# Kernel optimization log

Measured on AMD Instinct MI355X. Metric: run time of the kernel, lower is better.

The kernel has to match this reference:

```python
import jax, jax.numpy as jnp
import numpy as np

N = 65536
SIZES = [3, 256, 256, 256, 256, 1]
NU = np.float32(0.01 / np.pi)  # viscosity coefficient 0.01/pi


def setup_inputs() -> dict:
    key = jax.random.key(0)
    ks = jax.random.split(key, 16)
    inp = {
        "t": jax.random.uniform(ks[0], (N, 1), dtype=jnp.float32),
        "x": jax.random.uniform(ks[1], (N, 1), dtype=jnp.float32),
        "y": jax.random.uniform(ks[2], (N, 1), dtype=jnp.float32),
    }
    for i in range(len(SIZES) - 1):
        fan_in, fan_out = SIZES[i], SIZES[i + 1]
        scale = jnp.float32(1.0 / np.sqrt(fan_in))
        inp[f"W{i}"] = jax.random.normal(ks[3 + i], (fan_in, fan_out), dtype=jnp.float32) * scale
        inp[f"b{i}"] = jnp.zeros((fan_out,), dtype=jnp.float32)
    return inp


def reference(t, x, y, W0, b0, W1, b1, W2, b2, W3, b3, W4, b4):
    Ws = (W0, W1, W2, W3, W4)
    bs = (b0, b1, b2, b3, b4)

    def u_scalar(pt):  # pt: (3,) -> scalar u(t,x,y)
        h = pt
        for W, b in zip(Ws[:-1], bs[:-1]):
            h = jnp.tanh(h @ W + b)
        return (h @ Ws[-1] + bs[-1])[0]

    def point(pt):
        u, g = jax.value_and_grad(u_scalar)(pt)          # g = (u_t, u_x, u_y)
        H = jax.jacfwd(jax.grad(u_scalar))(pt)           # 3x3 Hessian (fwd-over-rev)
        f = g[0] + u * g[1] + u * g[2] - NU * (H[1, 1] + H[2, 2])
        return u, f

    pts = jnp.concatenate((t, x, y), axis=1)  # [N, 3]
    u, f = jax.vmap(point)(pts)
    return u[:, None], f[:, None]
```

## Files before the change

kernel.cpp:

```cpp
#include <hip/hip_runtime.h>

#define NPTS 65536
#define NU_F 0.0031830988618379067f

typedef __attribute__((ext_vector_type(8)))  _Float16 half8v;
typedef __attribute__((ext_vector_type(16))) float    f32x16;

__device__ __forceinline__ void jet5(float z, float zt, float zx, float zy, float zl,
                                     float& s0, float& s1, float& s2, float& s3, float& s4) {
    float e  = __expf(2.0f * z);
    float a  = 1.0f - 2.0f * __builtin_amdgcn_rcpf(e + 1.0f);
    float ap = 1.0f - a * a;
    float am = -2.0f * a * ap;
    s0 = a;
    s1 = ap * zt;
    s2 = ap * zx;
    s3 = ap * zy;
    s4 = ap * zl + am * (zx * zx + zy * zy);
}

__device__ __forceinline__ int swzoff(int sp, int byteInRow) {
    return (sp << 9) + (byteInRow ^ ((sp & 31) << 4));
}
union h4u { ushort4 u4; _Float16 h[4]; };
__device__ __forceinline__ void storeJ(char* baseB, int sp, int j0,
                                       _Float16 a0, _Float16 a1, _Float16 a2, _Float16 a3) {
    h4u v; v.h[0] = a0; v.h[1] = a1; v.h[2] = a2; v.h[3] = a3;
    *(ushort4*)(baseB + swzoff(sp, j0 * 2)) = v.u4;
}

__global__ __launch_bounds__(256)
void pinn_prep_kernel(const float* __restrict__ W1, const float* __restrict__ W2,
                      const float* __restrict__ W3, _Float16* __restrict__ ws) {
    int gid  = blockIdx.x * 256 + threadIdx.x;
    int l    = gid >> 13;
    int rem  = gid & 8191;
    int M    = rem >> 10;
    int kt   = (rem >> 6) & 15;
    int lane = rem & 63;
    const float* W = (l == 0) ? W1 : (l == 1) ? W2 : W3;
    int j  = M * 32 + (lane & 31);
    int k0 = kt * 16 + (lane >> 5) * 8;
    union { _Float16 h[8]; half8v v; } hf;
    #pragma unroll
    for (int jj = 0; jj < 8; ++jj)
        hf.h[jj] = (_Float16)W[(k0 + jj) * 256 + j];
    ((half8v*)ws)[l * 8192 + (M * 16 + kt) * 64 + lane] = hf.v;
}

__global__ __launch_bounds__(256, 2)
void pinn_burger2d_kernel(
    const float* __restrict__ t, const float* __restrict__ x, const float* __restrict__ y,
    const float* __restrict__ W0, const float* __restrict__ b0,
    const float* __restrict__ b1, const float* __restrict__ b2, const float* __restrict__ b3,
    const float* __restrict__ W4, const float* __restrict__ b4,
    const _Float16* __restrict__ wf, float* __restrict__ out)
{
    __shared__ _Float16 BjS[5 * 32 * 256];
    char* bjB = (char*)BjS;

    const int tid  = threadIdx.x;
    const int lane = tid & 63;
    const int wv   = tid >> 6;
    const int p    = lane & 31;
    const int kg   = lane >> 5;
    const int base = blockIdx.x * 32;
    const int gi   = base + p;

    const float tv = t[gi], xv = x[gi], yv = y[gi];

    #pragma unroll
    for (int m = 0; m < 2; ++m) {
        #pragma unroll
        for (int q = 0; q < 4; ++q) {
            const int j0 = wv * 64 + m * 32 + kg * 16 + q * 4;
            float4 w0t = *(const float4*)(W0 + j0);
            float4 w0x = *(const float4*)(W0 + 256 + j0);
            float4 w0y = *(const float4*)(W0 + 512 + j0);
            float4 bb  = *(const float4*)(b0 + j0);
            float wtA[4] = {w0t.x, w0t.y, w0t.z, w0t.w};
            float wxA[4] = {w0x.x, w0x.y, w0x.z, w0x.w};
            float wyA[4] = {w0y.x, w0y.y, w0y.z, w0y.w};
            float bbA[4] = {bb.x, bb.y, bb.z, bb.w};
            _Float16 h[5][4];
            #pragma unroll
            for (int i = 0; i < 4; ++i) {
                float z = tv * wtA[i] + xv * wxA[i] + yv * wyA[i] + bbA[i];
                float s0, s1, s2, s3, s4;
                jet5(z, wtA[i], wxA[i], wyA[i], 0.0f, s0, s1, s2, s3, s4);
                h[0][i] = (_Float16)s0; h[1][i] = (_Float16)s1; h[2][i] = (_Float16)s2;
                h[3][i] = (_Float16)s3; h[4][i] = (_Float16)s4;
            }
            #pragma unroll
            for (int s = 0; s < 5; ++s)
                storeJ(bjB, s * 32 + p, j0, h[s][0], h[s][1], h[s][2], h[s][3]);
        }
    }
    __syncthreads();

    f32x16 acc[2][5];

    for (int li = 0; li < 3; ++li) {
        #pragma unroll
        for (int m = 0; m < 2; ++m)
            #pragma unroll
            for (int c = 0; c < 5; ++c)
                acc[m][c] = (f32x16)(0.0f);

        const half8v* whf = (const half8v*)wf + li * 8192;

        #pragma unroll 4
        for (int kt = 0; kt < 16; ++kt) {
            const int bRow = kt * 32 + kg * 16;
            half8v bv0 = *(const half8v*)(bjB + swzoff(       p, bRow));
            half8v bv1 = *(const half8v*)(bjB + swzoff( 32 + p, bRow));
            half8v bv2 = *(const half8v*)(bjB + swzoff( 64 + p, bRow));
            half8v bv3 = *(const half8v*)(bjB + swzoff( 96 + p, bRow));
            half8v bv4 = *(const half8v*)(bjB + swzoff(128 + p, bRow));
            const int fa = (wv * 32 + kt) * 64 + lane;
            half8v whA = whf[fa];
            half8v whB = whf[fa + 1024];
            acc[0][0] = __builtin_amdgcn_mfma_f32_32x32x16_f16(whA, bv0, acc[0][0], 0, 0, 0);
            acc[0][1] = __builtin_amdgcn_mfma_f32_32x32x16_f16(whA, bv1, acc[0][1], 0, 0, 0);
            acc[0][2] = __builtin_amdgcn_mfma_f32_32x32x16_f16(whA, bv2, acc[0][2], 0, 0, 0);
            acc[0][3] = __builtin_amdgcn_mfma_f32_32x32x16_f16(whA, bv3, acc[0][3], 0, 0, 0);
            acc[0][4] = __builtin_amdgcn_mfma_f32_32x32x16_f16(whA, bv4, acc[0][4], 0, 0, 0);
            acc[1][0] = __builtin_amdgcn_mfma_f32_32x32x16_f16(whB, bv0, acc[1][0], 0, 0, 0);
            acc[1][1] = __builtin_amdgcn_mfma_f32_32x32x16_f16(whB, bv1, acc[1][1], 0, 0, 0);
            acc[1][2] = __builtin_amdgcn_mfma_f32_32x32x16_f16(whB, bv2, acc[1][2], 0, 0, 0);
            acc[1][3] = __builtin_amdgcn_mfma_f32_32x32x16_f16(whB, bv3, acc[1][3], 0, 0, 0);
            acc[1][4] = __builtin_amdgcn_mfma_f32_32x32x16_f16(whB, bv4, acc[1][4], 0, 0, 0);
        }
        __syncthreads();

        if (li < 2) {
            const float* bL = (li == 0) ? b1 : b2;
            #pragma unroll
            for (int m = 0; m < 2; ++m) {
                const int jt = (wv * 2 + m) * 32;
                #pragma unroll
                for (int q = 0; q < 4; ++q) {
                    const int j0 = jt + 8 * q + 4 * kg;
                    float4 bb = *(const float4*)(bL + j0);
                    float bbA[4] = {bb.x, bb.y, bb.z, bb.w};
                    _Float16 h[5][4];
                    #pragma unroll
                    for (int i = 0; i < 4; ++i) {
                        const int r = 4 * q + i;
                        float s0, s1, s2, s3, s4;
                        jet5(acc[m][0][r] + bbA[i], acc[m][1][r], acc[m][2][r],
                             acc[m][3][r], acc[m][4][r], s0, s1, s2, s3, s4);
                        h[0][i] = (_Float16)s0; h[1][i] = (_Float16)s1; h[2][i] = (_Float16)s2;
                        h[3][i] = (_Float16)s3; h[4][i] = (_Float16)s4;
                    }
                    #pragma unroll
                    for (int s = 0; s < 5; ++s)
                        storeJ(bjB, s * 32 + p, j0, h[s][0], h[s][1], h[s][2], h[s][3]);
                }
            }
            __syncthreads();
        }
    }

    float part[5] = {0, 0, 0, 0, 0};
    #pragma unroll
    for (int m = 0; m < 2; ++m) {
        const int jt = (wv * 2 + m) * 32;
        #pragma unroll
        for (int q = 0; q < 4; ++q) {
            const int j0 = jt + 8 * q + 4 * kg;
            float4 bb = *(const float4*)(b3 + j0);
            float4 w4 = *(const float4*)(W4 + j0);
            float bbA[4] = {bb.x, bb.y, bb.z, bb.w};
            float w4A[4] = {w4.x, w4.y, w4.z, w4.w};
            #pragma unroll
            for (int i = 0; i < 4; ++i) {
                const int r = 4 * q + i;
                float s0, s1, s2, s3, s4;
                jet5(acc[m][0][r] + bbA[i], acc[m][1][r], acc[m][2][r],
                     acc[m][3][r], acc[m][4][r], s0, s1, s2, s3, s4);
                part[0] += s0 * w4A[i];
                part[1] += s1 * w4A[i];
                part[2] += s2 * w4A[i];
                part[3] += s3 * w4A[i];
                part[4] += s4 * w4A[i];
            }
        }
    }
    #pragma unroll
    for (int s = 0; s < 5; ++s) part[s] += __shfl_xor(part[s], 32, 64);

    float* resf = (float*)BjS;
    if (lane < 32) {
        #pragma unroll
        for (int s = 0; s < 5; ++s) resf[(wv * 5 + s) * 32 + p] = part[s];
    }
    __syncthreads();

    if (tid < 32) {
        const int pp = tid;
        const int g  = base + pp;
        float u = b4[0], ut = 0, ux = 0, uy = 0, lap = 0;
        #pragma unroll
        for (int w = 0; w < 4; ++w) {
            u   += resf[(w * 5 + 0) * 32 + pp];
            ut  += resf[(w * 5 + 1) * 32 + pp];
            ux  += resf[(w * 5 + 2) * 32 + pp];
            uy  += resf[(w * 5 + 3) * 32 + pp];
            lap += resf[(w * 5 + 4) * 32 + pp];
        }
        out[g]        = u;
        out[NPTS + g] = ut + u * ux + u * uy - NU_F * lap;
    }
}

extern "C" void kernel_launch(void* const* d_in, const int* in_sizes, int n_in,
                              void* d_out, int out_size, void* d_ws, size_t ws_size,
                              hipStream_t stream) {
    const float* t  = (const float*)d_in[0];
    const float* x  = (const float*)d_in[1];
    const float* y  = (const float*)d_in[2];
    const float* W0 = (const float*)d_in[3];
    const float* b0 = (const float*)d_in[4];
    const float* W1 = (const float*)d_in[5];
    const float* b1 = (const float*)d_in[6];
    const float* W2 = (const float*)d_in[7];
    const float* b2 = (const float*)d_in[8];
    const float* W3 = (const float*)d_in[9];
    const float* b3 = (const float*)d_in[10];
    const float* W4 = (const float*)d_in[11];
    const float* b4 = (const float*)d_in[12];
    float* out = (float*)d_out;

    pinn_prep_kernel<<<96, 256, 0, stream>>>(W1, W2, W3, (_Float16*)d_ws);
    pinn_burger2d_kernel<<<NPTS / 32, 256, 0, stream>>>(
        t, x, y, W0, b0, b1, b2, b3, W4, b4, (const _Float16*)d_ws, out);
}
```

Baseline: 136.4 us.

## Switch to 16x16x32 MFMA with 16 points per block and higher occupancy

Each block now handles 16 points instead of 32, and the per-layer matmuls use 16x16x32 MFMA tiles with four output tiles per wave. The weight prepack is rewritten to match the new fragment layout. Shared memory and accumulator registers are halved, so launch bounds now target 4 blocks per CU. The cost is that each weight fragment loaded from global memory is reused over fewer points, roughly doubling weight traffic per point, and the final reduction needs an extra shuffle.

```diff
diff --git a/kernel.cpp b/kernel.cpp
--- a/kernel.cpp
+++ b/kernel.cpp
@@ -3,8 +3,8 @@
 #define NPTS 65536
 #define NU_F 0.0031830988618379067f
 
-typedef __attribute__((ext_vector_type(8)))  _Float16 half8v;
-typedef __attribute__((ext_vector_type(16))) float    f32x16;
+typedef __attribute__((ext_vector_type(8))) _Float16 half8v;
+typedef __attribute__((ext_vector_type(4))) float    f32x4;
 
 __device__ __forceinline__ void jet5(float z, float zt, float zx, float zy, float zl,
                                      float& s0, float& s1, float& s2, float& s3, float& s4) {
@@ -35,20 +35,20 @@
     int gid  = blockIdx.x * 256 + threadIdx.x;
     int l    = gid >> 13;
     int rem  = gid & 8191;
-    int M    = rem >> 10;
-    int kt   = (rem >> 6) & 15;
+    int M    = rem >> 9;
+    int kt   = (rem >> 6) & 7;
     int lane = rem & 63;
     const float* W = (l == 0) ? W1 : (l == 1) ? W2 : W3;
-    int j  = M * 32 + (lane & 31);
-    int k0 = kt * 16 + (lane >> 5) * 8;
+    int j  = M * 16 + (lane & 15);
+    int k0 = kt * 32 + (lane >> 4) * 8;
     union { _Float16 h[8]; half8v v; } hf;
     #pragma unroll
     for (int jj = 0; jj < 8; ++jj)
         hf.h[jj] = (_Float16)W[(k0 + jj) * 256 + j];
-    ((half8v*)ws)[l * 8192 + (M * 16 + kt) * 64 + lane] = hf.v;
-}
-
-__global__ __launch_bounds__(256, 2)
+    ((half8v*)ws)[l * 8192 + (M * 8 + kt) * 64 + lane] = hf.v;
+}
+
+__global__ __launch_bounds__(256, 4)
 void pinn_burger2d_kernel(
     const float* __restrict__ t, const float* __restrict__ x, const float* __restrict__ y,
     const float* __restrict__ W0, const float* __restrict__ b0,
@@ -56,107 +56,95 @@
     const float* __restrict__ W4, const float* __restrict__ b4,
     const _Float16* __restrict__ wf, float* __restrict__ out)
 {
-    __shared__ _Float16 BjS[5 * 32 * 256];
+    __shared__ _Float16 BjS[5 * 16 * 256];
     char* bjB = (char*)BjS;
 
     const int tid  = threadIdx.x;
     const int lane = tid & 63;
     const int wv   = tid >> 6;
-    const int p    = lane & 31;
-    const int kg   = lane >> 5;
-    const int base = blockIdx.x * 32;
+    const int p    = lane & 15;
+    const int quad = lane >> 4;
+    const int base = blockIdx.x * 16;
     const int gi   = base + p;
 
     const float tv = t[gi], xv = x[gi], yv = y[gi];
 
     #pragma unroll
-    for (int m = 0; m < 2; ++m) {
-        #pragma unroll
-        for (int q = 0; q < 4; ++q) {
-            const int j0 = wv * 64 + m * 32 + kg * 16 + q * 4;
-            float4 w0t = *(const float4*)(W0 + j0);
-            float4 w0x = *(const float4*)(W0 + 256 + j0);
-            float4 w0y = *(const float4*)(W0 + 512 + j0);
-            float4 bb  = *(const float4*)(b0 + j0);
-            float wtA[4] = {w0t.x, w0t.y, w0t.z, w0t.w};
-            float wxA[4] = {w0x.x, w0x.y, w0x.z, w0x.w};
-            float wyA[4] = {w0y.x, w0y.y, w0y.z, w0y.w};
-            float bbA[4] = {bb.x, bb.y, bb.z, bb.w};
-            _Float16 h[5][4];
-            #pragma unroll
-            for (int i = 0; i < 4; ++i) {
-                float z = tv * wtA[i] + xv * wxA[i] + yv * wyA[i] + bbA[i];
-                float s0, s1, s2, s3, s4;
-                jet5(z, wtA[i], wxA[i], wyA[i], 0.0f, s0, s1, s2, s3, s4);
-                h[0][i] = (_Float16)s0; h[1][i] = (_Float16)s1; h[2][i] = (_Float16)s2;
-                h[3][i] = (_Float16)s3; h[4][i] = (_Float16)s4;
-            }
-            #pragma unroll
-            for (int s = 0; s < 5; ++s)
-                storeJ(bjB, s * 32 + p, j0, h[s][0], h[s][1], h[s][2], h[s][3]);
-        }
+    for (int m = 0; m < 4; ++m) {
+        const int j0 = wv * 64 + m * 16 + quad * 4;
+        float4 w0t = *(const float4*)(W0 + j0);
+        float4 w0x = *(const float4*)(W0 + 256 + j0);
+        float4 w0y = *(const float4*)(W0 + 512 + j0);
+        float4 bb  = *(const float4*)(b0 + j0);
+        float wtA[4] = {w0t.x, w0t.y, w0t.z, w0t.w};
+        float wxA[4] = {w0x.x, w0x.y, w0x.z, w0x.w};
+        float wyA[4] = {w0y.x, w0y.y, w0y.z, w0y.w};
+        float bbA[4] = {bb.x, bb.y, bb.z, bb.w};
+        _Float16 h[5][4];
+        #pragma unroll
+        for (int i = 0; i < 4; ++i) {
+            float z = tv * wtA[i] + xv * wxA[i] + yv * wyA[i] + bbA[i];
+            float s0, s1, s2, s3, s4;
+            jet5(z, wtA[i], wxA[i], wyA[i], 0.0f, s0, s1, s2, s3, s4);
+            h[0][i] = (_Float16)s0; h[1][i] = (_Float16)s1; h[2][i] = (_Float16)s2;
+            h[3][i] = (_Float16)s3; h[4][i] = (_Float16)s4;
+        }
+        #pragma unroll
+        for (int s = 0; s < 5; ++s)
+            storeJ(bjB, s * 16 + p, j0, h[s][0], h[s][1], h[s][2], h[s][3]);
     }
     __syncthreads();
 
-    f32x16 acc[2][5];
+    f32x4 acc[4][5];
 
     for (int li = 0; li < 3; ++li) {
         #pragma unroll
-        for (int m = 0; m < 2; ++m)
+        for (int m = 0; m < 4; ++m)
             #pragma unroll
             for (int c = 0; c < 5; ++c)
-                acc[m][c] = (f32x16)(0.0f);
+                acc[m][c] = (f32x4)(0.0f);
 
         const half8v* whf = (const half8v*)wf + li * 8192;
 
-        #pragma unroll 4
-        for (int kt = 0; kt < 16; ++kt) {
-            const int bRow = kt * 32 + kg * 16;
-            half8v bv0 = *(const half8v*)(bjB + swzoff(       p, bRow));
-            half8v bv1 = *(const half8v*)(bjB + swzoff( 32 + p, bRow));
-            half8v bv2 = *(const half8v*)(bjB + swzoff( 64 + p, bRow));
-            half8v bv3 = *(const half8v*)(bjB + swzoff( 96 + p, bRow));
-            half8v bv4 = *(const half8v*)(bjB + swzoff(128 + p, bRow));
-            const int fa = (wv * 32 + kt) * 64 + lane;
-            half8v whA = whf[fa];
-            half8v whB = whf[fa + 1024];
-            acc[0][0] = __builtin_amdgcn_mfma_f32_32x32x16_f16(whA, bv0, acc[0][0], 0, 0, 0);
-            acc[0][1] = __builtin_amdgcn_mfma_f32_32x32x16_f16(whA, bv1, acc[0][1], 0, 0, 0);
-            acc[0][2] = __builtin_amdgcn_mfma_f32_32x32x16_f16(whA, bv2, acc[0][2], 0, 0, 0);
-            acc[0][3] = __builtin_amdgcn_mfma_f32_32x32x16_f16(whA, bv3, acc[0][3], 0, 0, 0);
-            acc[0][4] = __builtin_amdgcn_mfma_f32_32x32x16_f16(whA, bv4, acc[0][4], 0, 0, 0);
-            acc[1][0] = __builtin_amdgcn_mfma_f32_32x32x16_f16(whB, bv0, acc[1][0], 0, 0, 0);
-            acc[1][1] = __builtin_amdgcn_mfma_f32_32x32x16_f16(whB, bv1, acc[1][1], 0, 0, 0);
-            acc[1][2] = __builtin_amdgcn_mfma_f32_32x32x16_f16(whB, bv2, acc[1][2], 0, 0, 0);
-            acc[1][3] = __builtin_amdgcn_mfma_f32_32x32x16_f16(whB, bv3, acc[1][3], 0, 0, 0);
-            acc[1][4] = __builtin_amdgcn_mfma_f32_32x32x16_f16(whB, bv4, acc[1][4], 0, 0, 0);
+        #pragma unroll 2
+        for (int kt = 0; kt < 8; ++kt) {
+            const int bRow = kt * 64 + quad * 16;
+            half8v bv0 = *(const half8v*)(bjB + swzoff(     p, bRow));
+            half8v bv1 = *(const half8v*)(bjB + swzoff(16 + p, bRow));
+            half8v bv2 = *(const half8v*)(bjB + swzoff(32 + p, bRow));
+            half8v bv3 = *(const half8v*)(bjB + swzoff(48 + p, bRow));
+            half8v bv4 = *(const half8v*)(bjB + swzoff(64 + p, bRow));
+            #pragma unroll
+            for (int m = 0; m < 4; ++m) {
+                half8v wh = whf[((wv * 4 + m) * 8 + kt) * 64 + lane];
+                acc[m][0] = __builtin_amdgcn_mfma_f32_16x16x32_f16(wh, bv0, acc[m][0], 0, 0, 0);
+                acc[m][1] = __builtin_amdgcn_mfma_f32_16x16x32_f16(wh, bv1, acc[m][1], 0, 0, 0);
+                acc[m][2] = __builtin_amdgcn_mfma_f32_16x16x32_f16(wh, bv2, acc[m][2], 0, 0, 0);
+                acc[m][3] = __builtin_amdgcn_mfma_f32_16x16x32_f16(wh, bv3, acc[m][3], 0, 0, 0);
+                acc[m][4] = __builtin_amdgcn_mfma_f32_16x16x32_f16(wh, bv4, acc[m][4], 0, 0, 0);
+            }
         }
         __syncthreads();
 
         if (li < 2) {
             const float* bL = (li == 0) ? b1 : b2;
             #pragma unroll
-            for (int m = 0; m < 2; ++m) {
-                const int jt = (wv * 2 + m) * 32;
+            for (int m = 0; m < 4; ++m) {
+                const int j0 = (wv * 4 + m) * 16 + quad * 4;
+                float4 bb = *(const float4*)(bL + j0);
+                float bbA[4] = {bb.x, bb.y, bb.z, bb.w};
+                _Float16 h[5][4];
                 #pragma unroll
-                for (int q = 0; q < 4; ++q) {
-                    const int j0 = jt + 8 * q + 4 * kg;
-                    float4 bb = *(const float4*)(bL + j0);
-                    float bbA[4] = {bb.x, bb.y, bb.z, bb.w};
-                    _Float16 h[5][4];
-                    #pragma unroll
-                    for (int i = 0; i < 4; ++i) {
-                        const int r = 4 * q + i;
-                        float s0, s1, s2, s3, s4;
-                        jet5(acc[m][0][r] + bbA[i], acc[m][1][r], acc[m][2][r],
-                             acc[m][3][r], acc[m][4][r], s0, s1, s2, s3, s4);
-                        h[0][i] = (_Float16)s0; h[1][i] = (_Float16)s1; h[2][i] = (_Float16)s2;
-                        h[3][i] = (_Float16)s3; h[4][i] = (_Float16)s4;
-                    }
-                    #pragma unroll
-                    for (int s = 0; s < 5; ++s)
-                        storeJ(bjB, s * 32 + p, j0, h[s][0], h[s][1], h[s][2], h[s][3]);
+                for (int i = 0; i < 4; ++i) {
+                    float s0, s1, s2, s3, s4;
+                    jet5(acc[m][0][i] + bbA[i], acc[m][1][i], acc[m][2][i],
+                         acc[m][3][i], acc[m][4][i], s0, s1, s2, s3, s4);
+                    h[0][i] = (_Float16)s0; h[1][i] = (_Float16)s1; h[2][i] = (_Float16)s2;
+                    h[3][i] = (_Float16)s3; h[4][i] = (_Float16)s4;
                 }
+                #pragma unroll
+                for (int s = 0; s < 5; ++s)
+                    storeJ(bjB, s * 16 + p, j0, h[s][0], h[s][1], h[s][2], h[s][3]);
             }
             __syncthreads();
         }
@@ -164,50 +152,48 @@
 
     float part[5] = {0, 0, 0, 0, 0};
     #pragma unroll
-    for (int m = 0; m < 2; ++m) {
-        const int jt = (wv * 2 + m) * 32;
-        #pragma unroll
-        for (int q = 0; q < 4; ++q) {
-            const int j0 = jt + 8 * q + 4 * kg;
-            float4 bb = *(const float4*)(b3 + j0);
-            float4 w4 = *(const float4*)(W4 + j0);
-            float bbA[4] = {bb.x, bb.y, bb.z, bb.w};
-            float w4A[4] = {w4.x, w4.y, w4.z, w4.w};
-            #pragma unroll
-            for (int i = 0; i < 4; ++i) {
-                const int r = 4 * q + i;
-                float s0, s1, s2, s3, s4;
-                jet5(acc[m][0][r] + bbA[i], acc[m][1][r], acc[m][2][r],
-                     acc[m][3][r], acc[m][4][r], s0, s1, s2, s3, s4);
-                part[0] += s0 * w4A[i];
-                part[1] += s1 * w4A[i];
-                part[2] += s2 * w4A[i];
-                part[3] += s3 * w4A[i];
-                part[4] += s4 * w4A[i];
-            }
-        }
-    }
-    #pragma unroll
-    for (int s = 0; s < 5; ++s) part[s] += __shfl_xor(part[s], 32, 64);
+    for (int m = 0; m < 4; ++m) {
+        const int j0 = (wv * 4 + m) * 16 + quad * 4;
+        float4 bb = *(const float4*)(b3 + j0);
+        float4 w4 = *(const float4*)(W4 + j0);
+        float bbA[4] = {bb.x, bb.y, bb.z, bb.w};
+        float w4A[4] = {w4.x, w4.y, w4.z, w4.w};
+        #pragma unroll
+        for (int i = 0; i < 4; ++i) {
+            float s0, s1, s2, s3, s4;
+            jet5(acc[m][0][i] + bbA[i], acc[m][1][i], acc[m][2][i],
+                 acc[m][3][i], acc[m][4][i], s0, s1, s2, s3, s4);
+            part[0] += s0 * w4A[i];
+            part[1] += s1 * w4A[i];
+            part[2] += s2 * w4A[i];
+            part[3] += s3 * w4A[i];
+            part[4] += s4 * w4A[i];
+        }
+    }
+    #pragma unroll
+    for (int s = 0; s < 5; ++s) {
+        part[s] += __shfl_xor(part[s], 16, 64);
+        part[s] += __shfl_xor(part[s], 32, 64);
+    }
 
     float* resf = (float*)BjS;
-    if (lane < 32) {
-        #pragma unroll
-        for (int s = 0; s < 5; ++s) resf[(wv * 5 + s) * 32 + p] = part[s];
+    if (lane < 16) {
+        #pragma unroll
+        for (int s = 0; s < 5; ++s) resf[(wv * 5 + s) * 16 + p] = part[s];
     }
     __syncthreads();
 
-    if (tid < 32) {
+    if (tid < 16) {
         const int pp = tid;
         const int g  = base + pp;
         float u = b4[0], ut = 0, ux = 0, uy = 0, lap = 0;
         #pragma unroll
         for (int w = 0; w < 4; ++w) {
-            u   += resf[(w * 5 + 0) * 32 + pp];
-            ut  += resf[(w * 5 + 1) * 32 + pp];
-            ux  += resf[(w * 5 + 2) * 32 + pp];
-            uy  += resf[(w * 5 + 3) * 32 + pp];
-            lap += resf[(w * 5 + 4) * 32 + pp];
+            u   += resf[(w * 5 + 0) * 16 + pp];
+            ut  += resf[(w * 5 + 1) * 16 + pp];
+            ux  += resf[(w * 5 + 2) * 16 + pp];
+            uy  += resf[(w * 5 + 3) * 16 + pp];
+            lap += resf[(w * 5 + 4) * 16 + pp];
         }
         out[g]        = u;
         out[NPTS + g] = ut + u * ux + u * uy - NU_F * lap;
@@ -233,6 +219,6 @@
     float* out = (float*)d_out;
 
     pinn_prep_kernel<<<96, 256, 0, stream>>>(W1, W2, W3, (_Float16*)d_ws);
-    pinn_burger2d_kernel<<<NPTS / 32, 256, 0, stream>>>(
+    pinn_burger2d_kernel<<<NPTS / 16, 256, 0, stream>>>(
         t, x, y, W0, b0, b1, b2, b3, W4, b4, (const _Float16*)d_ws, out);
 }
```

New measurement: 146.9 us. 1.08x slower.

## Split output tiles across 8 waves per block and pack fp16 stores

Applied to the files above, without the earlier changes.

The point-block kernel now runs 8 waves of 512 threads instead of 4, and each wave owns one 32-column output tile instead of two. This halves the accumulator registers per wave and raises the number of waves that can hide MFMA and LDS latency. It also packs fp16 conversions with cvt_pkrtz, simplifies the second-derivative term of the tanh jet, and raises wave priority around the MFMA issue. In exchange, each block synchronises more waves, and the final reduction sums eight partials instead of four.

```diff
diff --git a/kernel.cpp b/kernel.cpp
--- a/kernel.cpp
+++ b/kernel.cpp
@@ -4,29 +4,34 @@
 #define NU_F 0.0031830988618379067f
 
 typedef __attribute__((ext_vector_type(8)))  _Float16 half8v;
+typedef __attribute__((ext_vector_type(2)))  __fp16   fp16x2;
 typedef __attribute__((ext_vector_type(16))) float    f32x16;
+
+__device__ __forceinline__ unsigned pk2(float a, float b) {
+    union { fp16x2 h; unsigned u; } c;
+    c.h = __builtin_amdgcn_cvt_pkrtz(a, b);
+    return c.u;
+}
 
 __device__ __forceinline__ void jet5(float z, float zt, float zx, float zy, float zl,
                                      float& s0, float& s1, float& s2, float& s3, float& s4) {
     float e  = __expf(2.0f * z);
     float a  = 1.0f - 2.0f * __builtin_amdgcn_rcpf(e + 1.0f);
     float ap = 1.0f - a * a;
-    float am = -2.0f * a * ap;
     s0 = a;
     s1 = ap * zt;
     s2 = ap * zx;
     s3 = ap * zy;
-    s4 = ap * zl + am * (zx * zx + zy * zy);
+    float q = zx * zx + zy * zy;
+    s4 = ap * __builtin_fmaf(-2.0f * a, q, zl);
 }
 
 __device__ __forceinline__ int swzoff(int sp, int byteInRow) {
     return (sp << 9) + (byteInRow ^ ((sp & 31) << 4));
 }
-union h4u { ushort4 u4; _Float16 h[4]; };
-__device__ __forceinline__ void storeJ(char* baseB, int sp, int j0,
-                                       _Float16 a0, _Float16 a1, _Float16 a2, _Float16 a3) {
-    h4u v; v.h[0] = a0; v.h[1] = a1; v.h[2] = a2; v.h[3] = a3;
-    *(ushort4*)(baseB + swzoff(sp, j0 * 2)) = v.u4;
+__device__ __forceinline__ void storeJ2(char* baseB, int sp, int j0,
+                                        unsigned lo, unsigned hi) {
+    *(uint2*)(baseB + swzoff(sp, j0 * 2)) = make_uint2(lo, hi);
 }
 
 __global__ __launch_bounds__(256)
@@ -48,7 +53,7 @@
     ((half8v*)ws)[l * 8192 + (M * 16 + kt) * 64 + lane] = hf.v;
 }
 
-__global__ __launch_bounds__(256, 2)
+__global__ __launch_bounds__(512, 2)
 void pinn_burger2d_kernel(
     const float* __restrict__ t, const float* __restrict__ x, const float* __restrict__ y,
     const float* __restrict__ W0, const float* __restrict__ b0,
@@ -70,93 +75,74 @@
     const float tv = t[gi], xv = x[gi], yv = y[gi];
 
     #pragma unroll
-    for (int m = 0; m < 2; ++m) {
-        #pragma unroll
-        for (int q = 0; q < 4; ++q) {
-            const int j0 = wv * 64 + m * 32 + kg * 16 + q * 4;
-            float4 w0t = *(const float4*)(W0 + j0);
-            float4 w0x = *(const float4*)(W0 + 256 + j0);
-            float4 w0y = *(const float4*)(W0 + 512 + j0);
-            float4 bb  = *(const float4*)(b0 + j0);
-            float wtA[4] = {w0t.x, w0t.y, w0t.z, w0t.w};
-            float wxA[4] = {w0x.x, w0x.y, w0x.z, w0x.w};
-            float wyA[4] = {w0y.x, w0y.y, w0y.z, w0y.w};
-            float bbA[4] = {bb.x, bb.y, bb.z, bb.w};
-            _Float16 h[5][4];
-            #pragma unroll
-            for (int i = 0; i < 4; ++i) {
-                float z = tv * wtA[i] + xv * wxA[i] + yv * wyA[i] + bbA[i];
-                float s0, s1, s2, s3, s4;
-                jet5(z, wtA[i], wxA[i], wyA[i], 0.0f, s0, s1, s2, s3, s4);
-                h[0][i] = (_Float16)s0; h[1][i] = (_Float16)s1; h[2][i] = (_Float16)s2;
-                h[3][i] = (_Float16)s3; h[4][i] = (_Float16)s4;
-            }
-            #pragma unroll
-            for (int s = 0; s < 5; ++s)
-                storeJ(bjB, s * 32 + p, j0, h[s][0], h[s][1], h[s][2], h[s][3]);
-        }
+    for (int q = 0; q < 4; ++q) {
+        const int j0 = wv * 32 + kg * 16 + q * 4;
+        float4 w0t = *(const float4*)(W0 + j0);
+        float4 w0x = *(const float4*)(W0 + 256 + j0);
+        float4 w0y = *(const float4*)(W0 + 512 + j0);
+        float4 bb  = *(const float4*)(b0 + j0);
+        float wtA[4] = {w0t.x, w0t.y, w0t.z, w0t.w};
+        float wxA[4] = {w0x.x, w0x.y, w0x.z, w0x.w};
+        float wyA[4] = {w0y.x, w0y.y, w0y.z, w0y.w};
+        float bbA[4] = {bb.x, bb.y, bb.z, bb.w};
+        float ss[5][4];
+        #pragma unroll
+        for (int i = 0; i < 4; ++i) {
+            float z = tv * wtA[i] + xv * wxA[i] + yv * wyA[i] + bbA[i];
+            jet5(z, wtA[i], wxA[i], wyA[i], 0.0f,
+                 ss[0][i], ss[1][i], ss[2][i], ss[3][i], ss[4][i]);
+        }
+        #pragma unroll
+        for (int s = 0; s < 5; ++s)
+            storeJ2(bjB, s * 32 + p, j0, pk2(ss[s][0], ss[s][1]), pk2(ss[s][2], ss[s][3]));
     }
     __syncthreads();
 
-    f32x16 acc[2][5];
+    f32x16 acc[5];
 
     for (int li = 0; li < 3; ++li) {
         #pragma unroll
-        for (int m = 0; m < 2; ++m)
-            #pragma unroll
-            for (int c = 0; c < 5; ++c)
-                acc[m][c] = (f32x16)(0.0f);
+        for (int c = 0; c < 5; ++c)
+            acc[c] = (f32x16)(0.0f);
 
         const half8v* whf = (const half8v*)wf + li * 8192;
 
         #pragma unroll 4
         for (int kt = 0; kt < 16; ++kt) {
             const int bRow = kt * 32 + kg * 16;
-            half8v bv0 = *(const half8v*)(bjB + swzoff(       p, bRow));
+            half8v bv0 = *(const half8v*)(bjB + swzoff(      p, bRow));
             half8v bv1 = *(const half8v*)(bjB + swzoff( 32 + p, bRow));
             half8v bv2 = *(const half8v*)(bjB + swzoff( 64 + p, bRow));
             half8v bv3 = *(const half8v*)(bjB + swzoff( 96 + p, bRow));
             half8v bv4 = *(const half8v*)(bjB + swzoff(128 + p, bRow));
-            const int fa = (wv * 32 + kt) * 64 + lane;
-            half8v whA = whf[fa];
-            half8v whB = whf[fa + 1024];
-            acc[0][0] = __builtin_amdgcn_mfma_f32_32x32x16_f16(whA, bv0, acc[0][0], 0, 0, 0);
-            acc[0][1] = __builtin_amdgcn_mfma_f32_32x32x16_f16(whA, bv1, acc[0][1], 0, 0, 0);
-            acc[0][2] = __builtin_amdgcn_mfma_f32_32x32x16_f16(whA, bv2, acc[0][2], 0, 0, 0);
-            acc[0][3] = __builtin_amdgcn_mfma_f32_32x32x16_f16(whA, bv3, acc[0][3], 0, 0, 0);
-            acc[0][4] = __builtin_amdgcn_mfma_f32_32x32x16_f16(whA, bv4, acc[0][4], 0, 0, 0);
-            acc[1][0] = __builtin_amdgcn_mfma_f32_32x32x16_f16(whB, bv0, acc[1][0], 0, 0, 0);
-            acc[1][1] = __builtin_amdgcn_mfma_f32_32x32x16_f16(whB, bv1, acc[1][1], 0, 0, 0);
-            acc[1][2] = __builtin_amdgcn_mfma_f32_32x32x16_f16(whB, bv2, acc[1][2], 0, 0, 0);
-            acc[1][3] = __builtin_amdgcn_mfma_f32_32x32x16_f16(whB, bv3, acc[1][3], 0, 0, 0);
-            acc[1][4] = __builtin_amdgcn_mfma_f32_32x32x16_f16(whB, bv4, acc[1][4], 0, 0, 0);
+            half8v wh  = whf[(wv * 16 + kt) * 64 + lane];
+            __builtin_amdgcn_s_setprio(1);
+            acc[0] = __builtin_amdgcn_mfma_f32_32x32x16_f16(wh, bv0, acc[0], 0, 0, 0);
+            acc[1] = __builtin_amdgcn_mfma_f32_32x32x16_f16(wh, bv1, acc[1], 0, 0, 0);
+            acc[2] = __builtin_amdgcn_mfma_f32_32x32x16_f16(wh, bv2, acc[2], 0, 0, 0);
+            acc[3] = __builtin_amdgcn_mfma_f32_32x32x16_f16(wh, bv3, acc[3], 0, 0, 0);
+            acc[4] = __builtin_amdgcn_mfma_f32_32x32x16_f16(wh, bv4, acc[4], 0, 0, 0);
+            __builtin_amdgcn_s_setprio(0);
         }
         __syncthreads();
 
         if (li < 2) {
             const float* bL = (li == 0) ? b1 : b2;
             #pragma unroll
-            for (int m = 0; m < 2; ++m) {
-                const int jt = (wv * 2 + m) * 32;
+            for (int q = 0; q < 4; ++q) {
+                const int j0 = wv * 32 + 8 * q + 4 * kg;
+                float4 bb = *(const float4*)(bL + j0);
+                float bbA[4] = {bb.x, bb.y, bb.z, bb.w};
+                float ss[5][4];
                 #pragma unroll
-                for (int q = 0; q < 4; ++q) {
-                    const int j0 = jt + 8 * q + 4 * kg;
-                    float4 bb = *(const float4*)(bL + j0);
-                    float bbA[4] = {bb.x, bb.y, bb.z, bb.w};
-                    _Float16 h[5][4];
-                    #pragma unroll
-                    for (int i = 0; i < 4; ++i) {
-                        const int r = 4 * q + i;
-                        float s0, s1, s2, s3, s4;
-                        jet5(acc[m][0][r] + bbA[i], acc[m][1][r], acc[m][2][r],
-                             acc[m][3][r], acc[m][4][r], s0, s1, s2, s3, s4);
-                        h[0][i] = (_Float16)s0; h[1][i] = (_Float16)s1; h[2][i] = (_Float16)s2;
-                        h[3][i] = (_Float16)s3; h[4][i] = (_Float16)s4;
-                    }
-                    #pragma unroll
-                    for (int s = 0; s < 5; ++s)
-                        storeJ(bjB, s * 32 + p, j0, h[s][0], h[s][1], h[s][2], h[s][3]);
+                for (int i = 0; i < 4; ++i) {
+                    const int r = 4 * q + i;
+                    jet5(acc[0][r] + bbA[i], acc[1][r], acc[2][r], acc[3][r], acc[4][r],
+                         ss[0][i], ss[1][i], ss[2][i], ss[3][i], ss[4][i]);
                 }
+                #pragma unroll
+                for (int s = 0; s < 5; ++s)
+                    storeJ2(bjB, s * 32 + p, j0, pk2(ss[s][0], ss[s][1]), pk2(ss[s][2], ss[s][3]));
             }
             __syncthreads();
         }
@@ -164,27 +150,23 @@
 
     float part[5] = {0, 0, 0, 0, 0};
     #pragma unroll
-    for (int m = 0; m < 2; ++m) {
-        const int jt = (wv * 2 + m) * 32;
-        #pragma unroll
-        for (int q = 0; q < 4; ++q) {
-            const int j0 = jt + 8 * q + 4 * kg;
-            float4 bb = *(const float4*)(b3 + j0);
-            float4 w4 = *(const float4*)(W4 + j0);
-            float bbA[4] = {bb.x, bb.y, bb.z, bb.w};
-            float w4A[4] = {w4.x, w4.y, w4.z, w4.w};
-            #pragma unroll
-            for (int i = 0; i < 4; ++i) {
-                const int r = 4 * q + i;
-                float s0, s1, s2, s3, s4;
-                jet5(acc[m][0][r] + bbA[i], acc[m][1][r], acc[m][2][r],
-                     acc[m][3][r], acc[m][4][r], s0, s1, s2, s3, s4);
-                part[0] += s0 * w4A[i];
-                part[1] += s1 * w4A[i];
-                part[2] += s2 * w4A[i];
-                part[3] += s3 * w4A[i];
-                part[4] += s4 * w4A[i];
-            }
+    for (int q = 0; q < 4; ++q) {
+        const int j0 = wv * 32 + 8 * q + 4 * kg;
+        float4 bb = *(const float4*)(b3 + j0);
+        float4 w4 = *(const float4*)(W4 + j0);
+        float bbA[4] = {bb.x, bb.y, bb.z, bb.w};
+        float w4A[4] = {w4.x, w4.y, w4.z, w4.w};
+        #pragma unroll
+        for (int i = 0; i < 4; ++i) {
+            const int r = 4 * q + i;
+            float s0, s1, s2, s3, s4;
+            jet5(acc[0][r] + bbA[i], acc[1][r], acc[2][r], acc[3][r], acc[4][r],
+                 s0, s1, s2, s3, s4);
+            part[0] += s0 * w4A[i];
+            part[1] += s1 * w4A[i];
+            part[2] += s2 * w4A[i];
+            part[3] += s3 * w4A[i];
+            part[4] += s4 * w4A[i];
         }
     }
     #pragma unroll
@@ -202,7 +184,7 @@
         const int g  = base + pp;
         float u = b4[0], ut = 0, ux = 0, uy = 0, lap = 0;
         #pragma unroll
-        for (int w = 0; w < 4; ++w) {
+        for (int w = 0; w < 8; ++w) {
             u   += resf[(w * 5 + 0) * 32 + pp];
             ut  += resf[(w * 5 + 1) * 32 + pp];
             ux  += resf[(w * 5 + 2) * 32 + pp];
@@ -233,6 +215,6 @@
     float* out = (float*)d_out;
 
     pinn_prep_kernel<<<96, 256, 0, stream>>>(W1, W2, W3, (_Float16*)d_ws);
-    pinn_burger2d_kernel<<<NPTS / 32, 256, 0, stream>>>(
+    pinn_burger2d_kernel<<<NPTS / 32, 512, 0, stream>>>(
         t, x, y, W0, b0, b1, b2, b3, W4, b4, (const _Float16*)d_ws, out);
 }
```

Measured after the change: 161.6 us. 18.5% more time.
